# Kernel optimization log

Measured on AMD Instinct MI355X. Metric: run time of the kernel, lower is better.

The kernel has to match this reference:

```python
import jax, jax.numpy as jnp
import numpy as np

D_MODEL, N_HEADS, D_FF = 1024, 16, 2752
B, S = 2, 2048
EPS = 1e-5


def setup_inputs() -> dict:
    key = jax.random.key(0)
    ks = jax.random.split(key, 8)
    def w(k, fan_in, fan_out):
        std = np.sqrt(2.0 / (fan_in + fan_out))
        return jax.random.truncated_normal(k, -3.0, 3.0, (fan_in, fan_out), jnp.float32) * std
    return {
        "x": jax.random.normal(ks[0], (B, S, D_MODEL), jnp.float32),
        "g1": jnp.ones((D_MODEL,), jnp.float32),
        "g2": jnp.ones((D_MODEL,), jnp.float32),
        "w_q": w(ks[1], D_MODEL, D_MODEL),
        "w_k": w(ks[2], D_MODEL, D_MODEL),
        "w_v": w(ks[3], D_MODEL, D_MODEL),
        "w_o": w(ks[4], D_MODEL, D_MODEL),
        "w1": w(ks[5], D_MODEL, D_FF),
        "w2": w(ks[6], D_FF, D_MODEL),
        "w3": w(ks[7], D_MODEL, D_FF),
    }


def rmsnorm(x, g):
    xf = x.astype(jnp.float32)
    rms = jnp.sqrt(jnp.mean(xf * xf, axis=-1, keepdims=True) + EPS)
    return (xf / rms).astype(x.dtype) * g


def reference(x, g1, g2, w_q, w_k, w_v, w_o, w1, w2, w3):
    b, s, d = x.shape
    h = N_HEADS
    dh = d // h

    # --- causal multi-head self-attention on norm1(x) ---
    xn = rmsnorm(x, g1)
    q = (xn @ w_q).reshape(b, s, h, dh).transpose(0, 2, 1, 3)  # b h s d
    k = (xn @ w_k).reshape(b, s, h, dh).transpose(0, 2, 1, 3)
    v = (xn @ w_v).reshape(b, s, h, dh).transpose(0, 2, 1, 3)

    scores = jnp.einsum('bhqd,bhkd->bhqk', q, k) / jnp.sqrt(jnp.float32(dh))
    causal = jnp.tril(jnp.ones((s, s), dtype=bool))
    scores = jnp.where(causal, scores, -jnp.inf)
    probs = jax.nn.softmax(scores, axis=-1)
    attn = jnp.einsum('bhqk,bhkd->bhqd', probs, v)
    attn = attn.transpose(0, 2, 1, 3).reshape(b, s, d)
    h_res = x + attn @ w_o

    # --- SwiGLU FFN on norm2(h) ---
    hn = rmsnorm(h_res, g2)
    x1 = hn @ w1
    gate = x1 * jax.nn.sigmoid(x1)
    ffn = (gate * (hn @ w3)) @ w2
    return h_res + ffn
```

## Files before the change

kernel.cpp:

```cpp
#include <hip/hip_runtime.h>
#include <hip/hip_bf16.h>

typedef unsigned short u16;
typedef __bf16 bf16x8 __attribute__((ext_vector_type(8)));
typedef float  f32x4  __attribute__((ext_vector_type(4)));

#define D_MODEL 1024
#define SEQ     2048
#define NHEAD   16
#define DHEAD   64
#define QKVS    3072

__device__ __forceinline__ float bflo(unsigned u) { return __uint_as_float(u << 16); }
__device__ __forceinline__ float bfhi(unsigned u) { return __uint_as_float(u & 0xffff0000u); }
__device__ __forceinline__ u16 f2bf(float f) {
    unsigned u = __float_as_uint(f);
    u += 0x7fffu + ((u >> 16) & 1u);
    return (u16)(u >> 16);
}
__device__ __forceinline__ u16 f2bf_fast(float f) {
    return (u16)((__float_as_uint(f) + 0x8000u) >> 16);
}
__device__ __forceinline__ void gld_lds16(const u16* g, u16* l) {
    __builtin_amdgcn_global_load_lds((const __attribute__((address_space(1))) void*)g,
                                     (__attribute__((address_space(3))) void*)l, 16, 0, 0);
}

__global__ void detect_k(const unsigned* __restrict__ g1w, int* __restrict__ flag) {
    int c = 0;
#pragma unroll
    for (int i = 0; i < 8; ++i) c += (g1w[i] == 0x3F800000u) ? 1 : 0;
    *flag = (c >= 4) ? 1 : 0;
}

__global__ __launch_bounds__(256) void tp_k(const void* __restrict__ in_, u16* __restrict__ out,
                                            int K, int N, const int* __restrict__ flagp) {
    __shared__ u16 tile[32][33];
    const int f32 = *flagp;
    int k0 = blockIdx.x * 32, n0 = blockIdx.y * 32;
    int tx = threadIdx.x & 31, ty = threadIdx.x >> 5;
#pragma unroll
    for (int i = 0; i < 32; i += 8) {
        int nn = n0 + tx;
        u16 v = 0;
        if (nn < N) {
            size_t idx = (size_t)(k0 + ty + i) * N + nn;
            v = f32 ? f2bf(((const float*)in_)[idx]) : ((const u16*)in_)[idx];
        }
        tile[ty + i][tx] = v;
    }
    __syncthreads();
#pragma unroll
    for (int i = 0; i < 32; i += 8)
        out[(size_t)(n0 + ty + i) * K + (k0 + tx)] = tile[tx][ty + i];
}

__global__ __launch_bounds__(256) void rms_k(const void* __restrict__ x_, const void* __restrict__ g_,
                                             u16* __restrict__ o, const int* __restrict__ flagp,
                                             int x_raw) {
    const size_t row = blockIdx.x;
    const int f32 = *flagp;
    const int xf32 = f32 & x_raw;
    int t = threadIdx.x;
    float f0, f1, f2, f3, g0, g1, g2, g3;
    if (xf32) {
        float4 xv = *(const float4*)((const float*)x_ + row * D_MODEL + t * 4);
        f0 = xv.x; f1 = xv.y; f2 = xv.z; f3 = xv.w;
    } else {
        uint2 u = *(const uint2*)((const u16*)x_ + row * D_MODEL + t * 4);
        f0 = bflo(u.x); f1 = bfhi(u.x); f2 = bflo(u.y); f3 = bfhi(u.y);
    }
    if (f32) {
        float4 gv = *(const float4*)((const float*)g_ + t * 4);
        g0 = gv.x; g1 = gv.y; g2 = gv.z; g3 = gv.w;
    } else {
        uint2 gu = *(const uint2*)((const u16*)g_ + t * 4);
        g0 = bflo(gu.x); g1 = bfhi(gu.x); g2 = bflo(gu.y); g3 = bfhi(gu.y);
    }
    float s = f0 * f0 + f1 * f1 + f2 * f2 + f3 * f3;
#pragma unroll
    for (int off = 32; off > 0; off >>= 1) s += __shfl_xor(s, off, 64);
    __shared__ float ps[4];
    if ((t & 63) == 0) ps[t >> 6] = s;
    __syncthreads();
    float tot = ps[0] + ps[1] + ps[2] + ps[3];
    float rinv = rsqrtf(tot * (1.0f / D_MODEL) + 1e-5f);
    float fv[4] = {f0, f1, f2, f3};
    float gv2[4] = {g0, g1, g2, g3};
    u16 r[4];
#pragma unroll
    for (int i = 0; i < 4; ++i)
        r[i] = f2bf(fv[i] * rinv * gv2[i]);
    uint2 w;
    w.x = (unsigned)r[0] | ((unsigned)r[1] << 16);
    w.y = (unsigned)r[2] | ((unsigned)r[3] << 16);
    *(uint2*)(o + row * D_MODEL + t * 4) = w;
}

__global__ __launch_bounds__(256) void gemm_k(const u16* __restrict__ A, int lda,
                                              const u16* __restrict__ Bt, int ldb,
                                              u16* C, int ldc,
                                              const void* res, int K, int mode,
                                              const int* __restrict__ flagp, int res_raw,
                                              int out32) {
    __shared__ alignas(16) u16 As[128 * 32];
    __shared__ alignas(16) u16 Bs[128 * 32];
    const int t = threadIdx.x;
    const int rf32 = (mode == 1 && res_raw) ? *flagp : 0;
    const int wid = t >> 6, lane = t & 63;
    const int wm = (wid >> 1) * 64, wn = (wid & 1) * 64;
    const int m0 = blockIdx.x * 128, n0 = blockIdx.y * 128;
    const int fr = lane & 15, quad = lane >> 4;

    f32x4 acc[4][4] = {};

    for (int k0 = 0; k0 < K; k0 += 32) {
        __syncthreads();
#pragma unroll
        for (int r = 0; r < 2; ++r) {
            int e = r * 256 + t;
            int row = e >> 2, c = (e & 3) * 8;
            gld_lds16(A  + (size_t)(m0 + row) * lda + k0 + c, As + e * 8);
            gld_lds16(Bt + (size_t)(n0 + row) * ldb + k0 + c, Bs + e * 8);
        }
        __syncthreads();
        bf16x8 af[4], bfr[4];
#pragma unroll
        for (int i = 0; i < 4; ++i) {
            af[i]  = *(const bf16x8*)(As + (wm + i * 16 + fr) * 32 + quad * 8);
            bfr[i] = *(const bf16x8*)(Bs + (wn + i * 16 + fr) * 32 + quad * 8);
        }
#pragma unroll
        for (int i = 0; i < 4; ++i)
#pragma unroll
            for (int j = 0; j < 4; ++j)
                acc[i][j] = __builtin_amdgcn_mfma_f32_16x16x32_bf16(af[i], bfr[j], acc[i][j], 0, 0, 0);
    }

#pragma unroll
    for (int i = 0; i < 4; ++i)
#pragma unroll
        for (int j = 0; j < 4; ++j)
#pragma unroll
            for (int r2 = 0; r2 < 4; ++r2) {
                int row = m0 + wm + i * 16 + quad * 4 + r2;
                int col = n0 + wn + j * 16 + fr;
                size_t idx = (size_t)row * ldc + col;
                float v = acc[i][j][r2];
                if (mode == 1) {
                    float rv = rf32 ? ((const float*)res)[idx]
                                    : __uint_as_float((unsigned)((const u16*)res)[idx] << 16);
                    v += rv;
                }
                if (out32) ((float*)C)[idx] = v;
                else       C[idx] = f2bf(v);
            }
}

__global__ __launch_bounds__(256) void gemm64_k(const u16* __restrict__ A, int lda,
                                                const u16* __restrict__ Bt, int ldb,
                                                u16* C, int ldc,
                                                const void* res, int K, int mode,
                                                const int* __restrict__ flagp, int res_raw,
                                                int out32) {
    __shared__ alignas(16) u16 As[64 * 32];
    __shared__ alignas(16) u16 Bs[128 * 32];
    const int t = threadIdx.x;
    const int rf32 = (mode == 1 && res_raw) ? *flagp : 0;
    const int wid = t >> 6, lane = t & 63;
    const int wm = (wid >> 1) * 32, wn = (wid & 1) * 64;
    const int m0 = blockIdx.x * 64, n0 = blockIdx.y * 128;
    const int fr = lane & 15, quad = lane >> 4;

    f32x4 acc[2][4] = {};

    for (int k0 = 0; k0 < K; k0 += 32) {
        __syncthreads();
        {
            int row = t >> 2, c = (t & 3) * 8;
            gld_lds16(A + (size_t)(m0 + row) * lda + k0 + c, As + t * 8);
        }
#pragma unroll
        for (int r = 0; r < 2; ++r) {
            int e = r * 256 + t;
            int row = e >> 2, c = (e & 3) * 8;
            gld_lds16(Bt + (size_t)(n0 + row) * ldb + k0 + c, Bs + e * 8);
        }
        __syncthreads();
        bf16x8 af[2], bfr[4];
#pragma unroll
        for (int i = 0; i < 2; ++i)
            af[i] = *(const bf16x8*)(As + (wm + i * 16 + fr) * 32 + quad * 8);
#pragma unroll
        for (int j = 0; j < 4; ++j)
            bfr[j] = *(const bf16x8*)(Bs + (wn + j * 16 + fr) * 32 + quad * 8);
#pragma unroll
        for (int i = 0; i < 2; ++i)
#pragma unroll
            for (int j = 0; j < 4; ++j)
                acc[i][j] = __builtin_amdgcn_mfma_f32_16x16x32_bf16(af[i], bfr[j], acc[i][j], 0, 0, 0);
    }

#pragma unroll
    for (int i = 0; i < 2; ++i)
#pragma unroll
        for (int j = 0; j < 4; ++j)
#pragma unroll
            for (int r2 = 0; r2 < 4; ++r2) {
                int row = m0 + wm + i * 16 + quad * 4 + r2;
                int col = n0 + wn + j * 16 + fr;
                size_t idx = (size_t)row * ldc + col;
                float v = acc[i][j][r2];
                if (mode == 1) {
                    float rv = rf32 ? ((const float*)res)[idx]
                                    : __uint_as_float((unsigned)((const u16*)res)[idx] << 16);
                    v += rv;
                }
                if (out32) ((float*)C)[idx] = v;
                else       C[idx] = f2bf(v);
            }
}

__global__ __launch_bounds__(256, 2) void ffn_k(const u16* __restrict__ A,
                                                const u16* __restrict__ B1t,
                                                const u16* __restrict__ B3t,
                                                u16* __restrict__ G, int ldg) {
    __shared__ alignas(16) u16 As[128 * 32];
    __shared__ alignas(16) u16 B1s[128 * 32];
    __shared__ alignas(16) u16 B3s[128 * 32];
    const int t = threadIdx.x;
    const int wid = t >> 6, lane = t & 63;
    const int wm = (wid >> 1) * 64, wn = (wid & 1) * 64;
    const int m0 = blockIdx.x * 128, n0 = blockIdx.y * 128;
    const int fr = lane & 15, quad = lane >> 4;

    f32x4 acc1[4][4] = {};
    f32x4 acc3[4][4] = {};

    for (int k0 = 0; k0 < 1024; k0 += 32) {
        __syncthreads();
#pragma unroll
        for (int r = 0; r < 2; ++r) {
            int e = r * 256 + t;
            int row = e >> 2, c = (e & 3) * 8;
            gld_lds16(A   + (size_t)(m0 + row) * 1024 + k0 + c, As  + e * 8);
            gld_lds16(B1t + (size_t)(n0 + row) * 1024 + k0 + c, B1s + e * 8);
            gld_lds16(B3t + (size_t)(n0 + row) * 1024 + k0 + c, B3s + e * 8);
        }
        __syncthreads();
        bf16x8 af[4], b1[4], b3[4];
#pragma unroll
        for (int i = 0; i < 4; ++i) {
            af[i] = *(const bf16x8*)(As  + (wm + i * 16 + fr) * 32 + quad * 8);
            b1[i] = *(const bf16x8*)(B1s + (wn + i * 16 + fr) * 32 + quad * 8);
            b3[i] = *(const bf16x8*)(B3s + (wn + i * 16 + fr) * 32 + quad * 8);
        }
#pragma unroll
        for (int i = 0; i < 4; ++i)
#pragma unroll
            for (int j = 0; j < 4; ++j) {
                acc1[i][j] = __builtin_amdgcn_mfma_f32_16x16x32_bf16(af[i], b1[j], acc1[i][j], 0, 0, 0);
                acc3[i][j] = __builtin_amdgcn_mfma_f32_16x16x32_bf16(af[i], b3[j], acc3[i][j], 0, 0, 0);
            }
    }

#pragma unroll
    for (int i = 0; i < 4; ++i)
#pragma unroll
        for (int j = 0; j < 4; ++j)
#pragma unroll
            for (int r2 = 0; r2 < 4; ++r2) {
                int row = m0 + wm + i * 16 + quad * 4 + r2;
                int col = n0 + wn + j * 16 + fr;
                float xv = acc1[i][j][r2];
                xv = fminf(fmaxf(xv, -60.f), 60.f);
                float sg = xv / (1.0f + __expf(-xv));
                G[(size_t)row * ldg + col] = f2bf(sg * acc3[i][j][r2]);
            }
}

__global__ __launch_bounds__(256) void vtp_k(const u16* __restrict__ qkv, u16* __restrict__ vt) {
    __shared__ u16 tile[32][33];
    const int bh = blockIdx.z, b = bh >> 4, h = bh & 15;
    const int s0 = blockIdx.x * 32, d0 = blockIdx.y * 32;
    const int tx = threadIdx.x & 31, ty = threadIdx.x >> 5;
#pragma unroll
    for (int i = 0; i < 32; i += 8)
        tile[ty + i][tx] = qkv[(size_t)(b * SEQ + s0 + ty + i) * QKVS + 2048 + h * 64 + d0 + tx];
    __syncthreads();
#pragma unroll
    for (int i = 0; i < 32; i += 8)
        vt[(size_t)(bh * 64 + d0 + ty + i) * SEQ + s0 + tx] = tile[tx][ty + i];
}

#define KPAD 68
#define PPAD 72
__global__ __launch_bounds__(256) void fattn_k(const u16* __restrict__ QKV, const u16* __restrict__ Vt,
                                               u16* __restrict__ O) {
    __shared__ alignas(16) u16 Ks[64 * KPAD];
    __shared__ alignas(16) u16 Vs[64 * KPAD];
    __shared__ alignas(16) u16 Ps[4 * 32 * PPAD];

    const int bh = blockIdx.y;
    const size_t baseqk = ((size_t)(bh >> 4) * SEQ) * QKVS + (size_t)(bh & 15) * DHEAD;
    const size_t baseo  = ((size_t)(bh >> 4) * SEQ) * D_MODEL + (size_t)(bh & 15) * DHEAD;
    const size_t vtbase = (size_t)bh * 64 * SEQ;
    const u16* Qp = QKV + baseqk;
    const u16* Kp = QKV + baseqk + 1024;
    const int chunk = (gridDim.x - 1) - blockIdx.x;
    const int r0 = chunk * 128;
    const int t = threadIdx.x, w = t >> 6, lane = t & 63;
    const int fr = lane & 15, quad = lane >> 4;

    bf16x8 qa[2][2];
#pragma unroll
    for (int s = 0; s < 2; ++s) {
        const u16* qp = Qp + (size_t)(r0 + w * 32 + s * 16 + fr) * QKVS + quad * 8;
        qa[s][0] = *(const bf16x8*)(qp);
        qa[s][1] = *(const bf16x8*)(qp + 32);
    }

    f32x4 oacc[2][4] = {};
    float lp[2][4] = {};
    u16* Pw = Ps + w * 32 * PPAD;
    const float sc = 0.125f * 1.44269504f;
    const int qrow_min = r0 + w * 32;
    const int kend = r0 + 128;

    for (int kb = 0; kb < kend; kb += 64) {
        __syncthreads();
#pragma unroll
        for (int it = 0; it < 2; ++it) {
            int e = it * 256 + t;
            int rr = e >> 3, cc = (e & 7) * 8;
            *(uint4*)(Ks + rr * KPAD + cc) = *(const uint4*)(Kp + (size_t)(kb + rr) * QKVS + cc);
            *(uint4*)(Vs + rr * KPAD + cc) = *(const uint4*)(Vt + vtbase + (size_t)rr * SEQ + kb + cc);
        }
        __syncthreads();

#pragma unroll
        for (int s = 0; s < 2; ++s) {
            f32x4 sac[4] = {};
#pragma unroll
            for (int n = 0; n < 4; ++n) {
                bf16x8 kf0 = *(const bf16x8*)(Ks + (n * 16 + fr) * KPAD + quad * 8);
                bf16x8 kf1 = *(const bf16x8*)(Ks + (n * 16 + fr) * KPAD + 32 + quad * 8);
                sac[n] = __builtin_amdgcn_mfma_f32_16x16x32_bf16(qa[s][0], kf0, sac[n], 0, 0, 0);
                sac[n] = __builtin_amdgcn_mfma_f32_16x16x32_bf16(qa[s][1], kf1, sac[n], 0, 0, 0);
            }
            const int smin = qrow_min + s * 16;
            if (kb + 64 <= smin) {
#pragma unroll
                for (int n = 0; n < 4; ++n)
#pragma unroll
                    for (int r = 0; r < 4; ++r) {
                        float p = exp2f(fminf(sac[n][r] * sc, 126.f));
                        lp[s][r] += p;
                        Pw[(s * 16 + quad * 4 + r) * PPAD + n * 16 + fr] = f2bf_fast(p);
                    }
            } else {
                const int qb_s = smin + quad * 4;
#pragma unroll
                for (int n = 0; n < 4; ++n) {
                    int key = kb + n * 16 + fr;
#pragma unroll
                    for (int r = 0; r < 4; ++r) {
                        float p = (key <= qb_s + r) ? exp2f(fminf(sac[n][r] * sc, 126.f)) : 0.f;
                        lp[s][r] += p;
                        Pw[(s * 16 + quad * 4 + r) * PPAD + n * 16 + fr] = f2bf_fast(p);
                    }
                }
            }
        }
        __threadfence_block();
        bf16x8 vf0[4], vf1[4];
#pragma unroll
        for (int n = 0; n < 4; ++n) {
            vf0[n] = *(const bf16x8*)(Vs + (n * 16 + fr) * KPAD + quad * 8);
            vf1[n] = *(const bf16x8*)(Vs + (n * 16 + fr) * KPAD + 32 + quad * 8);
        }
#pragma unroll
        for (int s = 0; s < 2; ++s) {
            bf16x8 pa0 = *(const bf16x8*)(Pw + (s * 16 + fr) * PPAD + quad * 8);
            bf16x8 pa1 = *(const bf16x8*)(Pw + (s * 16 + fr) * PPAD + 32 + quad * 8);
#pragma unroll
            for (int n = 0; n < 4; ++n) {
                oacc[s][n] = __builtin_amdgcn_mfma_f32_16x16x32_bf16(pa0, vf0[n], oacc[s][n], 0, 0, 0);
                oacc[s][n] = __builtin_amdgcn_mfma_f32_16x16x32_bf16(pa1, vf1[n], oacc[s][n], 0, 0, 0);
            }
        }
    }

#pragma unroll
    for (int s = 0; s < 2; ++s)
#pragma unroll
        for (int r = 0; r < 4; ++r) {
            float v = lp[s][r];
            v += __shfl_xor(v, 1, 64);
            v += __shfl_xor(v, 2, 64);
            v += __shfl_xor(v, 4, 64);
            v += __shfl_xor(v, 8, 64);
            lp[s][r] = 1.0f / v;
        }
#pragma unroll
    for (int s = 0; s < 2; ++s)
#pragma unroll
        for (int r = 0; r < 4; ++r) {
            u16* op = O + baseo + (size_t)(qrow_min + s * 16 + quad * 4 + r) * D_MODEL;
#pragma unroll
            for (int n = 0; n < 4; ++n)
                op[n * 16 + fr] = f2bf(oacc[s][n][r] * lp[s][r]);
        }
}

extern "C" void kernel_launch(void* const* d_in, const int* in_sizes, int n_in,
                              void* d_out, int out_size, void* d_ws, size_t ws_size,
                              hipStream_t stream) {
    const void* x  = d_in[0];
    const void* g1 = d_in[1];
    const void* g2 = d_in[2];
    const void* wq = d_in[3];
    const void* wk = d_in[4];
    const void* wv = d_in[5];
    const void* wo = d_in[6];
    const void* w1 = d_in[7];
    const void* w2 = d_in[8];
    const void* w3 = d_in[9];
    u16* ws  = (u16*)d_ws;

    u16* xn    = ws;
    u16* qkv   = ws + 4194304;
    u16* gate  = ws + 4194304;
    u16* hres  = ws + 16777216;
    int* flag  = (int*)(ws + 20971520);
    u16* wqkvT = ws + 20971776;
    u16* woT   = ws + 20971776;
    u16* w2T   = ws + 20971776;
    u16* vt    = (u16*)d_out;
    u16* attn  = (u16*)d_out + 4194304;
    u16* w1T   = (u16*)d_out;
    u16* w3T   = (u16*)d_out + 2883584;

    detect_k<<<1, 1, 0, stream>>>((const unsigned*)g1, flag);

    tp_k<<<dim3(32, 32), 256, 0, stream>>>(wq, wqkvT,           1024, 1024, flag);
    tp_k<<<dim3(32, 32), 256, 0, stream>>>(wk, wqkvT + 1048576, 1024, 1024, flag);
    tp_k<<<dim3(32, 32), 256, 0, stream>>>(wv, wqkvT + 2097152, 1024, 1024, flag);
    rms_k<<<4096, 256, 0, stream>>>(x, g1, xn, flag, 1);

    gemm_k<<<dim3(32, 24), 256, 0, stream>>>(xn, 1024, wqkvT, 1024, qkv, QKVS, nullptr, 1024, 0, flag, 0, 0);

    tp_k<<<dim3(32, 32), 256, 0, stream>>>(wo, woT, 1024, 1024, flag);
    vtp_k<<<dim3(64, 2, 32), 256, 0, stream>>>(qkv, vt);
    fattn_k<<<dim3(16, 32), 256, 0, stream>>>(qkv, vt, attn);

    gemm64_k<<<dim3(64, 8), 256, 0, stream>>>(attn, 1024, woT, 1024, hres, 1024, x, 1024, 1, flag, 1, 0);

    rms_k<<<4096, 256, 0, stream>>>(hres, g2, xn, flag, 0);

    tp_k<<<dim3(32, 88), 256, 0, stream>>>(w1, w1T, 1024, 2752, flag);
    tp_k<<<dim3(32, 88), 256, 0, stream>>>(w3, w3T, 1024, 2752, flag);
    tp_k<<<dim3(86, 32), 256, 0, stream>>>(w2, w2T, 2752, 1024, flag);

    ffn_k<<<dim3(32, 22), 256, 0, stream>>>(xn, w1T, w3T, gate, 2816);

    gemm64_k<<<dim3(64, 8), 256, 0, stream>>>(gate, 2816, w2T, 2752, (u16*)d_out, 1024, hres, 2752, 1, flag, 0, 1);
}
```

Measured before the change: 441.6 us.

## Split long causal attention chunks across two blocks and batch weight transposes

Attention query chunks 8-15, which have the most key tiles, are split into two halves processed by separate blocks. Each half writes unnormalised bf16 partial outputs and row sums, and a new combine kernel adds them and normalises. This balances work across blocks in the causal grid. Separate weight transpose launches are also merged into batched z-indexed launches to cut launch overhead. The combine assumes both halves share a compatible softmax max reference, and it adds an extra pass plus bf16 rounding of the partials.

```diff
diff --git a/kernel.cpp b/kernel.cpp
--- a/kernel.cpp
+++ b/kernel.cpp
@@ -53,6 +53,32 @@
 #pragma unroll
     for (int i = 0; i < 32; i += 8)
         out[(size_t)(n0 + ty + i) * K + (k0 + tx)] = tile[tx][ty + i];
+}
+
+__global__ __launch_bounds__(256) void tpm_k(const void* __restrict__ a, const void* __restrict__ b,
+                                             const void* __restrict__ c, u16* __restrict__ out,
+                                             int K, int N, int outStride,
+                                             const int* __restrict__ flagp) {
+    __shared__ u16 tile[32][33];
+    const void* in_ = (blockIdx.z == 0) ? a : (blockIdx.z == 1) ? b : c;
+    u16* o = out + (size_t)blockIdx.z * outStride;
+    const int f32 = *flagp;
+    int k0 = blockIdx.x * 32, n0 = blockIdx.y * 32;
+    int tx = threadIdx.x & 31, ty = threadIdx.x >> 5;
+#pragma unroll
+    for (int i = 0; i < 32; i += 8) {
+        int nn = n0 + tx;
+        u16 v = 0;
+        if (nn < N) {
+            size_t idx = (size_t)(k0 + ty + i) * N + nn;
+            v = f32 ? f2bf(((const float*)in_)[idx]) : ((const u16*)in_)[idx];
+        }
+        tile[ty + i][tx] = v;
+    }
+    __syncthreads();
+#pragma unroll
+    for (int i = 0; i < 32; i += 8)
+        o[(size_t)(n0 + ty + i) * K + (k0 + tx)] = tile[tx][ty + i];
 }
 
 __global__ __launch_bounds__(256) void rms_k(const void* __restrict__ x_, const void* __restrict__ g_,
@@ -296,18 +322,30 @@
 #define KPAD 68
 #define PPAD 72
 __global__ __launch_bounds__(256) void fattn_k(const u16* __restrict__ QKV, const u16* __restrict__ Vt,
-                                               u16* __restrict__ O) {
+                                               u16* __restrict__ O, u16* __restrict__ pO,
+                                               float* __restrict__ pL) {
     __shared__ alignas(16) u16 Ks[64 * KPAD];
     __shared__ alignas(16) u16 Vs[64 * KPAD];
     __shared__ alignas(16) u16 Ps[4 * 32 * PPAD];
 
     const int bh = blockIdx.y;
+    const int j = blockIdx.x;
+    int chunk, kt0, ktn, partial, slot;
+    if (j < 16) {
+        chunk = 15 - (j >> 1);
+        int h = chunk + 1;
+        int half = j & 1;
+        kt0 = half * h; ktn = h; partial = 1;
+        slot = (bh << 4) + ((chunk - 8) << 1) + half;
+    } else {
+        chunk = 23 - j; kt0 = 0; ktn = 2 * (chunk + 1); partial = 0; slot = 0;
+    }
+
     const size_t baseqk = ((size_t)(bh >> 4) * SEQ) * QKVS + (size_t)(bh & 15) * DHEAD;
     const size_t baseo  = ((size_t)(bh >> 4) * SEQ) * D_MODEL + (size_t)(bh & 15) * DHEAD;
     const size_t vtbase = (size_t)bh * 64 * SEQ;
     const u16* Qp = QKV + baseqk;
     const u16* Kp = QKV + baseqk + 1024;
-    const int chunk = (gridDim.x - 1) - blockIdx.x;
     const int r0 = chunk * 128;
     const int t = threadIdx.x, w = t >> 6, lane = t & 63;
     const int fr = lane & 15, quad = lane >> 4;
@@ -325,9 +363,9 @@
     u16* Pw = Ps + w * 32 * PPAD;
     const float sc = 0.125f * 1.44269504f;
     const int qrow_min = r0 + w * 32;
-    const int kend = r0 + 128;
-
-    for (int kb = 0; kb < kend; kb += 64) {
+
+    for (int kt = kt0; kt < kt0 + ktn; ++kt) {
+        const int kb = kt * 64;
         __syncthreads();
 #pragma unroll
         for (int it = 0; it < 2; ++it) {
@@ -400,17 +438,49 @@
             v += __shfl_xor(v, 2, 64);
             v += __shfl_xor(v, 4, 64);
             v += __shfl_xor(v, 8, 64);
-            lp[s][r] = 1.0f / v;
-        }
-#pragma unroll
-    for (int s = 0; s < 2; ++s)
-#pragma unroll
-        for (int r = 0; r < 4; ++r) {
-            u16* op = O + baseo + (size_t)(qrow_min + s * 16 + quad * 4 + r) * D_MODEL;
-#pragma unroll
-            for (int n = 0; n < 4; ++n)
-                op[n * 16 + fr] = f2bf(oacc[s][n][r] * lp[s][r]);
-        }
+            lp[s][r] = v;
+        }
+    if (!partial) {
+#pragma unroll
+        for (int s = 0; s < 2; ++s)
+#pragma unroll
+            for (int r = 0; r < 4; ++r) {
+                float linv = 1.0f / lp[s][r];
+                u16* op = O + baseo + (size_t)(qrow_min + s * 16 + quad * 4 + r) * D_MODEL;
+#pragma unroll
+                for (int n = 0; n < 4; ++n)
+                    op[n * 16 + fr] = f2bf(oacc[s][n][r] * linv);
+            }
+    } else {
+        u16* po = pO + (size_t)slot * 8192;
+#pragma unroll
+        for (int s = 0; s < 2; ++s)
+#pragma unroll
+            for (int r = 0; r < 4; ++r) {
+                int rl = w * 32 + s * 16 + quad * 4 + r;
+#pragma unroll
+                for (int n = 0; n < 4; ++n)
+                    po[rl * 64 + n * 16 + fr] = f2bf(oacc[s][n][r]);
+                if (fr == 0) pL[slot * 128 + rl] = lp[s][r];
+            }
+    }
+}
+
+__global__ __launch_bounds__(256) void fcomb_k(const u16* __restrict__ pO, const float* __restrict__ pL,
+                                               u16* __restrict__ O) {
+    const int id = blockIdx.x;
+    const int bh = id >> 3, chunk = 8 + (id & 7);
+    const int s0 = (bh << 4) + ((chunk - 8) << 1);
+    const size_t baseo = ((size_t)(bh >> 4) * SEQ) * D_MODEL + (size_t)(bh & 15) * DHEAD;
+    const int r0 = chunk * 128;
+    const u16* p0 = pO + (size_t)s0 * 8192;
+    const u16* p1 = p0 + 8192;
+    for (int e = threadIdx.x; e < 8192; e += 256) {
+        int row = e >> 6, d = e & 63;
+        float o = __uint_as_float((unsigned)p0[e] << 16) + __uint_as_float((unsigned)p1[e] << 16);
+        float l = pL[s0 * 128 + row] + pL[(s0 + 1) * 128 + row];
+        O[baseo + (size_t)(r0 + row) * D_MODEL + d] = f2bf(o / l);
+    }
 }
 
 extern "C" void kernel_launch(void* const* d_in, const int* in_sizes, int n_in,
@@ -428,38 +498,38 @@
     const void* w3 = d_in[9];
     u16* ws  = (u16*)d_ws;
 
-    u16* xn    = ws;
-    u16* qkv   = ws + 4194304;
-    u16* gate  = ws + 4194304;
-    u16* hres  = ws + 16777216;
-    int* flag  = (int*)(ws + 20971520);
-    u16* wqkvT = ws + 20971776;
-    u16* woT   = ws + 20971776;
-    u16* w2T   = ws + 20971776;
-    u16* vt    = (u16*)d_out;
-    u16* attn  = (u16*)d_out + 4194304;
-    u16* w1T   = (u16*)d_out;
-    u16* w3T   = (u16*)d_out + 2883584;
+    u16*   xn    = ws;
+    float* pL    = (float*)ws;
+    u16*   qkv   = ws + 4194304;
+    u16*   gate  = ws + 4194304;
+    u16*   pO    = ws + 16777216;
+    u16*   hres  = ws + 16777216;
+    int*   flag  = (int*)(ws + 20971520);
+    u16*   wqkvT = ws + 20971776;
+    u16*   woT   = ws + 20971776;
+    u16*   w2T   = ws + 20971776;
+    u16*   vt    = (u16*)d_out;
+    u16*   attn  = (u16*)d_out + 4194304;
+    u16*   w1T   = (u16*)d_out;
+    u16*   w3T   = (u16*)d_out + 2883584;
 
     detect_k<<<1, 1, 0, stream>>>((const unsigned*)g1, flag);
 
-    tp_k<<<dim3(32, 32), 256, 0, stream>>>(wq, wqkvT,           1024, 1024, flag);
-    tp_k<<<dim3(32, 32), 256, 0, stream>>>(wk, wqkvT + 1048576, 1024, 1024, flag);
-    tp_k<<<dim3(32, 32), 256, 0, stream>>>(wv, wqkvT + 2097152, 1024, 1024, flag);
+    tpm_k<<<dim3(32, 32, 3), 256, 0, stream>>>(wq, wk, wv, wqkvT, 1024, 1024, 1048576, flag);
     rms_k<<<4096, 256, 0, stream>>>(x, g1, xn, flag, 1);
 
     gemm_k<<<dim3(32, 24), 256, 0, stream>>>(xn, 1024, wqkvT, 1024, qkv, QKVS, nullptr, 1024, 0, flag, 0, 0);
 
     tp_k<<<dim3(32, 32), 256, 0, stream>>>(wo, woT, 1024, 1024, flag);
     vtp_k<<<dim3(64, 2, 32), 256, 0, stream>>>(qkv, vt);
-    fattn_k<<<dim3(16, 32), 256, 0, stream>>>(qkv, vt, attn);
+    fattn_k<<<dim3(24, 32), 256, 0, stream>>>(qkv, vt, attn, pO, pL);
+    fcomb_k<<<256, 256, 0, stream>>>(pO, pL, attn);
 
     gemm64_k<<<dim3(64, 8), 256, 0, stream>>>(attn, 1024, woT, 1024, hres, 1024, x, 1024, 1, flag, 1, 0);
 
     rms_k<<<4096, 256, 0, stream>>>(hres, g2, xn, flag, 0);
 
-    tp_k<<<dim3(32, 88), 256, 0, stream>>>(w1, w1T, 1024, 2752, flag);
-    tp_k<<<dim3(32, 88), 256, 0, stream>>>(w3, w3T, 1024, 2752, flag);
+    tpm_k<<<dim3(32, 88, 2), 256, 0, stream>>>(w1, w3, w3, w1T, 1024, 2752, 2883584, flag);
     tp_k<<<dim3(86, 32), 256, 0, stream>>>(w2, w2T, 2752, 1024, flag);
 
     ffn_k<<<dim3(32, 22), 256, 0, stream>>>(xn, w1T, w3T, gate, 2816);
```

After: 438.8 us. About the same (-0.6%).
